# Kernel tuning notes

Measured on AMD Instinct MI355X. Metric: run time of the kernel, lower is better.

Reference implementation:

```python
import jax, jax.numpy as jnp
import numpy as np

B, D, H, W = 16, 512, 32, 32
K = 2048            # n_codes
BETA = 0.25
DECAY = 0.99
EPS = 1e-5


def _l2norm(x):
    # matches F.normalize(x, dim=-1) with eps=1e-12
    n = jnp.linalg.norm(x, axis=-1, keepdims=True)
    return x / jnp.maximum(n, 1e-12)


def setup_inputs() -> dict:
    key = jax.random.key(0)
    k1, k2, k3, k4 = jax.random.split(key, 4)
    z = jax.random.normal(k1, (B, D, H, W), dtype=jnp.float32)
    embeddings = jax.random.normal(k2, (K, D), dtype=jnp.float32) * (1.0 / K)
    N_buf = jax.random.uniform(k3, (K,), dtype=jnp.float32) + 0.5
    z_avg = jax.random.normal(k4, (K, D), dtype=jnp.float32) * (1.0 / K)
    return {"z": z, "embeddings": embeddings, "N_buf": N_buf, "z_avg": z_avg}


def reference(z, embeddings, N_buf, z_avg):
    b, d, h, w = z.shape
    # [B,C,H,W] -> [B,H,W,C] -> [N, D]
    flat = z.transpose(0, 2, 3, 1).reshape(-1, d)          # [N, D]
    z_norm = _l2norm(flat)                                  # [N, D]
    cb_norm = _l2norm(embeddings)                           # [K, D]

    # squared euclidean distances (kept in the same expanded form as source)
    distances = (jnp.sum(z_norm ** 2, axis=1, keepdims=True)
                 + jnp.sum(cb_norm ** 2, axis=1)
                 - 2.0 * jnp.matmul(z_norm, cb_norm.T))     # [N, K]
    distance_prob = jax.nn.softmax(-distances, axis=1)      # [N, K]
    encoding_indices = jnp.argmin(distances, axis=1)        # [N] int

    # NOTE: faithful to source -- gathers rows of z_norm (inputs), not codebook
    emb = z_norm[encoding_indices]                          # [N, D]

    # training-mode EMA statistics (one-hot matmul expressed as segment_sum)
    n_total = jax.ops.segment_sum(jnp.ones_like(encoding_indices, dtype=z.dtype),
                                  encoding_indices, num_segments=K)      # [K]
    encode_sum = jax.ops.segment_sum(z_norm, encoding_indices,
                                     num_segments=K)                     # [K, D]
    N_new = DECAY * N_buf + (1.0 - DECAY) * n_total
    z_avg_new = DECAY * z_avg + (1.0 - DECAY) * encode_sum
    n = jnp.sum(N_new)
    weights = (N_new + EPS) / (n + K * EPS) * n                          # [K]
    embeddings_new = z_avg_new / weights[:, None]                        # [K, D]

    commitment_loss = jnp.mean((z_norm - jax.lax.stop_gradient(emb)) ** 2)
    loss = BETA * commitment_loss
    codebook_sum = jnp.sum(jnp.abs(embeddings_new))

    q = emb.reshape(b, h, w, d).transpose(0, 3, 1, 2)       # [B, D, H, W]
    return (q, distance_prob, commitment_loss, loss, codebook_sum,
            embeddings_new, N_new, z_avg_new)
```

## Files before the change

### kernel.cpp

```cpp
#include <hip/hip_runtime.h>

#define NROW 16384
#define KC   2048
#define DIM  512

typedef __attribute__((ext_vector_type(8))) short  short8;
typedef __attribute__((ext_vector_type(4))) float  floatx4;


__device__ __forceinline__ unsigned short f2bf(float f) {
  unsigned int u = __float_as_uint(f);
  u += 0x7fffu + ((u >> 16) & 1u);
  return (unsigned short)(u >> 16);
}

#define GLDS(gsrc, ldst) __builtin_amdgcn_global_load_lds( \
    (const __attribute__((address_space(1))) unsigned int*)(gsrc), \
    (__attribute__((address_space(3))) unsigned int*)(ldst), 16, 0, 0)

__global__ void k_cbnorm(const float* __restrict__ emb,
                         unsigned short* __restrict__ cb_bf,
                         float* __restrict__ csq) {
  const int k = blockIdx.x;
  const int t = threadIdx.x;
  const float* row = emb + (size_t)k * DIM;
  float v0 = row[t], v1 = row[t + 256];
  float ss = v0 * v0 + v1 * v1;
#pragma unroll
  for (int o = 32; o; o >>= 1) ss += __shfl_xor(ss, o, 64);
  __shared__ float red[4];
  if ((t & 63) == 0) red[t >> 6] = ss;
  __syncthreads();
  float tot = red[0] + red[1] + red[2] + red[3];
  float r = 1.0f / fmaxf(sqrtf(tot), 1e-12f);
  cb_bf[(size_t)k * DIM + t]       = f2bf(v0 * r);
  cb_bf[(size_t)k * DIM + t + 256] = f2bf(v1 * r);
  if (t == 0) csq[k] = tot * r * r;
}

__global__ void k_pnorm(const float* __restrict__ z, float* __restrict__ rnorm) {
  const int b  = blockIdx.x;
  const int pc = blockIdx.y;
  const int tx = threadIdx.x & 63;
  const int ty = threadIdx.x >> 6;
  const int p  = pc * 64 + tx;
  const float* zp = z + (size_t)b * (DIM * 1024) + p;
  float ss = 0.f;
  for (int d = ty; d < DIM; d += 4) {
    float v = zp[(size_t)d * 1024];
    ss += v * v;
  }
  __shared__ float red[4][64];
  red[ty][tx] = ss;
  __syncthreads();
  if (ty == 0) {
    float tot = red[0][tx] + red[1][tx] + red[2][tx] + red[3][tx];
    rnorm[b * 1024 + p] = 1.0f / fmaxf(sqrtf(tot), 1e-12f);
  }
}

__global__ void k_transpose(const float* __restrict__ z, const float* __restrict__ rnorm,
                            float* __restrict__ flatT, unsigned short* __restrict__ zbf) {
  __shared__ float tile[32][33];
  __shared__ float srn[32];
  const int dt = blockIdx.x;
  const int pt = blockIdx.y;
  const int b  = blockIdx.z;
  const int tx = threadIdx.x & 31;
  const int ty = threadIdx.x >> 5;
  if (threadIdx.x < 32) srn[threadIdx.x] = rnorm[b * 1024 + pt * 32 + threadIdx.x];
  const size_t zb = (size_t)b * (DIM * 1024);
#pragma unroll
  for (int i = 0; i < 4; ++i) {
    int d = dt * 32 + ty + i * 8;
    int p = pt * 32 + tx;
    tile[ty + i * 8][tx] = z[zb + (size_t)d * 1024 + p];
  }
  __syncthreads();
#pragma unroll
  for (int i = 0; i < 4; ++i) {
    int p = pt * 32 + ty + i * 8;
    int d = dt * 32 + tx;
    float v = tile[tx][ty + i * 8];
    size_t o = (size_t)(b * 1024 + p) * DIM + d;
    flatT[o] = v;
    zbf[o]   = f2bf(v * srn[ty + i * 8]);
  }
}

__global__ __launch_bounds__(256) void k_gemm(const unsigned short* __restrict__ A,
                                              const unsigned short* __restrict__ Bm,
                                              const float* __restrict__ csq,
                                              float* __restrict__ T) {
  __shared__ alignas(16) unsigned short smA[128 * 64];
  __shared__ alignas(16) unsigned short smB[128 * 64];
  const int tid  = threadIdx.x;
  const int wid  = tid >> 6;
  const int lane = tid & 63;
  const int m0 = blockIdx.x * 128;
  const int n0 = blockIdx.y * 128;
  const int wm = (wid >> 1) * 64;
  const int wn = (wid & 1) * 64;

  floatx4 acc[4][4];
  const floatx4 z4 = {0.f, 0.f, 0.f, 0.f};
#pragma unroll
  for (int mi = 0; mi < 4; ++mi)
#pragma unroll
    for (int ni = 0; ni < 4; ++ni) acc[mi][ni] = z4;

  const int srow = tid >> 3;
  const int scol = (tid & 7) * 8;
  const unsigned short* Abase = A  + (size_t)(m0 + srow) * DIM + scol;
  const unsigned short* Bbase = Bm + (size_t)(n0 + srow) * DIM + scol;

  for (int kt = 0; kt < 8; ++kt) {
    const int kb = kt * 64;
#pragma unroll
    for (int i = 0; i < 4; ++i) {
      GLDS(Abase + kb + (size_t)i * 32 * DIM, &smA[i * 2048 + tid * 8]);
      GLDS(Bbase + kb + (size_t)i * 32 * DIM, &smB[i * 2048 + tid * 8]);
    }
    __syncthreads();
    const int q  = lane >> 4;
    const int mr = lane & 15;
#pragma unroll
    for (int kk = 0; kk < 2; ++kk) {
      const int cb = (kk * 4 + q) * 8;
      short8 af[4], bfr[4];
#pragma unroll
      for (int mi = 0; mi < 4; ++mi)
        af[mi] = *(const short8*)&smA[(wm + mi * 16 + mr) * 64 + cb];
#pragma unroll
      for (int ni = 0; ni < 4; ++ni)
        bfr[ni] = *(const short8*)&smB[(wn + ni * 16 + mr) * 64 + cb];
#pragma unroll
      for (int mi = 0; mi < 4; ++mi)
#pragma unroll
        for (int ni = 0; ni < 4; ++ni)
          acc[mi][ni] = __builtin_amdgcn_mfma_f32_16x16x32_bf16(af[mi], bfr[ni], acc[mi][ni], 0, 0, 0);
    }
    __syncthreads();
  }

  const int col = lane & 15;
  const int rq  = (lane >> 4) * 4;
  float csqv[4];
#pragma unroll
  for (int ni = 0; ni < 4; ++ni) csqv[ni] = csq[n0 + wn + ni * 16 + col];
#pragma unroll
  for (int mi = 0; mi < 4; ++mi)
#pragma unroll
    for (int r = 0; r < 4; ++r) {
      size_t rowoff = (size_t)(m0 + wm + mi * 16 + rq + r) * KC;
#pragma unroll
      for (int ni = 0; ni < 4; ++ni)
        T[rowoff + n0 + wn + ni * 16 + col] = 2.0f * acc[mi][ni][r] - csqv[ni];
    }
}

#define MARGIN_T 2.0e-2f

__global__ void k_row(float* __restrict__ T, const float* __restrict__ flatT,
                      const float* __restrict__ emb, const float* __restrict__ rnorm,
                      int* __restrict__ idx, float* __restrict__ enc_sum,
                      float* __restrict__ n_total, double* __restrict__ cl_part) {
  const int n = blockIdx.x;
  const int t = threadIdx.x;
  const int lane = t & 63;
  const int wid  = t >> 6;
  float* row = T + (size_t)n * KC;

  float tv[8];
  float mx = -3.4e38f;
#pragma unroll
  for (int j = 0; j < 8; ++j) {
    tv[j] = row[t + j * 256];
    mx = fmaxf(mx, tv[j]);
  }
#pragma unroll
  for (int o = 32; o; o >>= 1) mx = fmaxf(mx, __shfl_xor(mx, o, 64));
  __shared__ float redm[4];
  __shared__ float redsum[4];
  __shared__ int   s_cnt;
  __shared__ int   s_list[16];
  __shared__ int   s_j;
  if (t == 0) s_cnt = 0;
  if (lane == 0) redm[wid] = mx;
  __syncthreads();
  const float MX = fmaxf(fmaxf(redm[0], redm[1]), fmaxf(redm[2], redm[3]));
  float ev[8];
  float sum = 0.f;
#pragma unroll
  for (int j = 0; j < 8; ++j) {
    int k = t + j * 256;
    if (tv[j] >= MX - MARGIN_T) {
      int p = atomicAdd(&s_cnt, 1);
      if (p < 16) s_list[p] = k;
    }
    ev[j] = __expf(tv[j] - MX);
    sum += ev[j];
  }
#pragma unroll
  for (int o = 32; o; o >>= 1) sum += __shfl_xor(sum, o, 64);
  if (lane == 0) redsum[wid] = sum;
  __syncthreads();
  const float inv = 1.0f / (redsum[0] + redsum[1] + redsum[2] + redsum[3]);
#pragma unroll
  for (int j = 0; j < 8; ++j) row[t + j * 256] = ev[j] * inv;

  const int c = s_cnt;
  if (c == 1) {
    if (t == 0) s_j = s_list[0];
  } else if (wid == 0) {
    const float* zr = flatT + (size_t)n * DIM;
    double zs = 0.0;
    for (int d = lane; d < DIM; d += 64) { double v = zr[d]; zs += v * v; }
#pragma unroll
    for (int o = 32; o; o >>= 1) zs += __shfl_xor(zs, o, 64);
    double zn = fmax(sqrt(zs), 1e-12);
    double best = 1e300;
    int bestk = 0x7fffffff;
    const int m = (c > 16) ? KC : c;
    for (int ci = 0; ci < m; ++ci) {
      int k = (c > 16) ? ci : s_list[ci];
      const float* er = emb + (size_t)k * DIM;
      double cs = 0.0, dot = 0.0;
      for (int d = lane; d < DIM; d += 64) {
        double e = er[d], zv = zr[d];
        cs += e * e; dot += zv * e;
      }
#pragma unroll
      for (int o = 32; o; o >>= 1) { cs += __shfl_xor(cs, o, 64); dot += __shfl_xor(dot, o, 64); }
      double cn = fmax(sqrt(cs), 1e-12);
      double score = cs / (cn * cn) - 2.0 * dot / (zn * cn);
      if (score < best || (score == best && k < bestk)) { best = score; bestk = k; }
    }
    if (lane == 0) s_j = bestk;
  }
  __syncthreads();
  const int j = s_j;
  if (t == 0) idx[n] = j;

  const float rn = rnorm[n], rj = rnorm[j];
  const float* zr  = flatT + (size_t)n * DIM;
  const float* zjr = flatT + (size_t)j * DIM;
  double cl = 0.0;
#pragma unroll
  for (int i = 0; i < 2; ++i) {
    int d = t + i * 256;
    float zv  = zr[d] * rn;
    float evv = zjr[d] * rj;
    float df  = zv - evv;
    cl += (double)df * (double)df;
    atomicAdd(&enc_sum[(size_t)j * DIM + d], zv);
  }
#pragma unroll
  for (int o = 32; o; o >>= 1) cl += __shfl_xor(cl, o, 64);
  __shared__ double redd[4];
  if (lane == 0) redd[wid] = cl;
  __syncthreads();
  if (t == 0) {
    cl_part[n] = redd[0] + redd[1] + redd[2] + redd[3];
    atomicAdd(&n_total[j], 1.0f);
  }
}

__global__ void k_tail(const float* __restrict__ za, const float* __restrict__ es,
                       const float* __restrict__ Nb, const float* __restrict__ ntot,
                       float* __restrict__ out_zav, float* __restrict__ outN,
                       float* __restrict__ out_emb, double* __restrict__ cbs_part) {
  const int k = blockIdx.x;
  const int t = threadIdx.x;
  const int lane = t & 63, wid = t >> 6;
  float s = 0.f;
#pragma unroll
  for (int i = 0; i < 8; ++i) {
    int kk = t + i * 256;
    s += 0.99f * Nb[kk] + 0.01f * ntot[kk];
  }
#pragma unroll
  for (int o = 32; o; o >>= 1) s += __shfl_xor(s, o, 64);
  __shared__ float redn[4];
  if (lane == 0) redn[wid] = s;
  __syncthreads();
  const float nv = redn[0] + redn[1] + redn[2] + redn[3];
  const float Nn = 0.99f * Nb[k] + 0.01f * ntot[k];
  if (t == 0) outN[k] = Nn;
  const float w = (Nn + 1e-5f) / (nv + 0.02048f) * nv;
  double a = 0.0;
#pragma unroll
  for (int i = 0; i < 2; ++i) {
    size_t gi = (size_t)k * DIM + t + i * 256;
    float zv = 0.99f * za[gi] + 0.01f * es[gi];
    out_zav[gi] = zv;
    float e = zv / w;
    out_emb[gi] = e;
    a += (double)fabsf(e);
  }
#pragma unroll
  for (int o = 32; o; o >>= 1) a += __shfl_xor(a, o, 64);
  __shared__ double red[4];
  if (lane == 0) red[wid] = a;
  __syncthreads();
  if (t == 0) cbs_part[k] = red[0] + red[1] + red[2] + red[3];
}

__global__ void k_q(const float* __restrict__ flatT, const float* __restrict__ rnorm,
                    const int* __restrict__ idx, float* __restrict__ q) {
  const int o = blockIdx.x * 256 + threadIdx.x;
  const int b = o >> 19;
  const int d = (o >> 10) & 511;
  const int p = o & 1023;
  const int j = idx[(b << 10) + p];
  q[o] = flatT[(size_t)j * DIM + d] * rnorm[j];
}

__global__ void k_final(const double* __restrict__ cl_part, const double* __restrict__ cbs_part,
                        float* __restrict__ out) {
  const int t = threadIdx.x;
  double cl = 0.0, cb = 0.0;
  for (int i = t; i < NROW; i += 256) cl += cl_part[i];
  for (int i = t; i < KC; i += 256) cb += cbs_part[i];
#pragma unroll
  for (int o = 32; o; o >>= 1) { cl += __shfl_xor(cl, o, 64); cb += __shfl_xor(cb, o, 64); }
  __shared__ double redc[4], redb[4];
  if ((t & 63) == 0) { redc[t >> 6] = cl; redb[t >> 6] = cb; }
  __syncthreads();
  if (t == 0) {
    double clm = (redc[0] + redc[1] + redc[2] + redc[3]) / 8388608.0;
    double cbs = redb[0] + redb[1] + redb[2] + redb[3];
    out[41943040] = (float)clm;
    out[41943041] = (float)(0.25 * clm);
    out[41943042] = (float)cbs;
  }
}

extern "C" void kernel_launch(void* const* d_in, const int* in_sizes, int n_in,
                              void* d_out, int out_size, void* d_ws, size_t ws_size,
                              hipStream_t stream) {
  const float* z   = (const float*)d_in[0];
  const float* emb = (const float*)d_in[1];
  const float* Nb  = (const float*)d_in[2];
  const float* za  = (const float*)d_in[3];
  float* out = (float*)d_out;
  char*  ws  = (char*)d_ws;

  float*          flatT     = (float*)(ws + 0);
  unsigned short* cb_bf     = (unsigned short*)(ws + 33554432);
  float*          csq       = (float*)(ws + 35651584);
  float*          rnorm     = (float*)(ws + 35659776);
  int*            idx       = (int*)(ws + 35725312);
  double*         cl_part   = (double*)(ws + 35790848);
  double*         cbs_part  = (double*)(ws + 35921920);
  float*          enc_sum   = (float*)(ws + 35938304);
  float*          n_total   = (float*)(ws + 40132608);

  unsigned short* z_bf  = (unsigned short*)out;
  float* S        = out + 8388608;
  float* out_emb  = out + 41943043;
  float* out_N    = out + 42991619;
  float* out_zav  = out + 42993667;

  hipMemsetAsync(ws + 35938304, 0, 4202496, stream);

  k_cbnorm   <<<KC, 256, 0, stream>>>(emb, cb_bf, csq);
  k_pnorm    <<<dim3(16, 16), 256, 0, stream>>>(z, rnorm);
  k_transpose<<<dim3(16, 32, 16), 256, 0, stream>>>(z, rnorm, flatT, z_bf);
  k_gemm     <<<dim3(NROW / 128, KC / 128), 256, 0, stream>>>(z_bf, cb_bf, csq, S);
  k_row      <<<NROW, 256, 0, stream>>>(S, flatT, emb, rnorm, idx, enc_sum, n_total, cl_part);
  k_tail     <<<KC, 256, 0, stream>>>(za, enc_sum, Nb, n_total, out_zav, out_N, out_emb, cbs_part);
  k_q        <<<32768, 256, 0, stream>>>(flatT, rnorm, idx, out);
  k_final    <<<1, 256, 0, stream>>>(cl_part, cbs_part, out);
}
```

Measured before the change: 468.1 us.

## Use fixed softmax shift, split row kernel, merge small kernels

The softmax kernel now exponentiates with a fixed shift of 1, relying on normalized vectors bounding logits, so max and sum reduce together in one pass with vectorized float4 loads and stores. Candidate selection uses a multiplicative threshold on exponentials and writes candidates to global memory. A separate pick kernel then handles argmin refinement and accumulation. The codebook and pixel norm kernels are merged into one launch, and the final reduction is folded into an extra block of the q kernel. This trades one extra launch and extra global traffic for fewer barriers and better-coalesced softmax access.

```diff
diff --git a/kernel.cpp b/kernel.cpp
--- a/kernel.cpp
+++ b/kernel.cpp
@@ -18,44 +18,47 @@
     (const __attribute__((address_space(1))) unsigned int*)(gsrc), \
     (__attribute__((address_space(3))) unsigned int*)(ldst), 16, 0, 0)
 
-__global__ void k_cbnorm(const float* __restrict__ emb,
-                         unsigned short* __restrict__ cb_bf,
-                         float* __restrict__ csq) {
-  const int k = blockIdx.x;
-  const int t = threadIdx.x;
-  const float* row = emb + (size_t)k * DIM;
-  float v0 = row[t], v1 = row[t + 256];
-  float ss = v0 * v0 + v1 * v1;
-#pragma unroll
-  for (int o = 32; o; o >>= 1) ss += __shfl_xor(ss, o, 64);
-  __shared__ float red[4];
-  if ((t & 63) == 0) red[t >> 6] = ss;
-  __syncthreads();
-  float tot = red[0] + red[1] + red[2] + red[3];
-  float r = 1.0f / fmaxf(sqrtf(tot), 1e-12f);
-  cb_bf[(size_t)k * DIM + t]       = f2bf(v0 * r);
-  cb_bf[(size_t)k * DIM + t + 256] = f2bf(v1 * r);
-  if (t == 0) csq[k] = tot * r * r;
-}
-
-__global__ void k_pnorm(const float* __restrict__ z, float* __restrict__ rnorm) {
-  const int b  = blockIdx.x;
-  const int pc = blockIdx.y;
-  const int tx = threadIdx.x & 63;
-  const int ty = threadIdx.x >> 6;
-  const int p  = pc * 64 + tx;
-  const float* zp = z + (size_t)b * (DIM * 1024) + p;
-  float ss = 0.f;
-  for (int d = ty; d < DIM; d += 4) {
-    float v = zp[(size_t)d * 1024];
-    ss += v * v;
-  }
-  __shared__ float red[4][64];
-  red[ty][tx] = ss;
-  __syncthreads();
-  if (ty == 0) {
-    float tot = red[0][tx] + red[1][tx] + red[2][tx] + red[3][tx];
-    rnorm[b * 1024 + p] = 1.0f / fmaxf(sqrtf(tot), 1e-12f);
+__global__ void k_prep(const float* __restrict__ emb,
+                       unsigned short* __restrict__ cb_bf,
+                       float* __restrict__ csq,
+                       const float* __restrict__ z,
+                       float* __restrict__ rnorm) {
+  __shared__ float red4[4];
+  __shared__ float redp[4][64];
+  if (blockIdx.x < KC) {
+    const int k = blockIdx.x;
+    const int t = threadIdx.x;
+    const float* row = emb + (size_t)k * DIM;
+    float v0 = row[t], v1 = row[t + 256];
+    float ss = v0 * v0 + v1 * v1;
+#pragma unroll
+    for (int o = 32; o; o >>= 1) ss += __shfl_xor(ss, o, 64);
+    if ((t & 63) == 0) red4[t >> 6] = ss;
+    __syncthreads();
+    float tot = red4[0] + red4[1] + red4[2] + red4[3];
+    float r = 1.0f / fmaxf(sqrtf(tot), 1e-12f);
+    cb_bf[(size_t)k * DIM + t]       = f2bf(v0 * r);
+    cb_bf[(size_t)k * DIM + t + 256] = f2bf(v1 * r);
+    if (t == 0) csq[k] = tot * r * r;
+  } else {
+    const int blk = blockIdx.x - KC;
+    const int b  = blk >> 4;
+    const int pc = blk & 15;
+    const int tx = threadIdx.x & 63;
+    const int ty = threadIdx.x >> 6;
+    const int p  = pc * 64 + tx;
+    const float* zp = z + (size_t)b * (DIM * 1024) + p;
+    float ss = 0.f;
+    for (int d = ty; d < DIM; d += 4) {
+      float v = zp[(size_t)d * 1024];
+      ss += v * v;
+    }
+    redp[ty][tx] = ss;
+    __syncthreads();
+    if (ty == 0) {
+      float tot = redp[0][tx] + redp[1][tx] + redp[2][tx] + redp[3][tx];
+      rnorm[b * 1024 + p] = 1.0f / fmaxf(sqrtf(tot), 1e-12f);
+    }
   }
 }
 
@@ -159,59 +162,69 @@
     }
 }
 
-#define MARGIN_T 2.0e-2f
-
-__global__ void k_row(float* __restrict__ T, const float* __restrict__ flatT,
-                      const float* __restrict__ emb, const float* __restrict__ rnorm,
-                      int* __restrict__ idx, float* __restrict__ enc_sum,
-                      float* __restrict__ n_total, double* __restrict__ cl_part) {
+#define EXP_MARGIN 0.980198673f
+
+__global__ void k_softmax(float* __restrict__ T,
+                          int* __restrict__ cand_cnt, int* __restrict__ cand_list) {
   const int n = blockIdx.x;
   const int t = threadIdx.x;
-  const int lane = t & 63;
-  const int wid  = t >> 6;
+  const int lane = t & 63, wid = t >> 6;
   float* row = T + (size_t)n * KC;
-
-  float tv[8];
-  float mx = -3.4e38f;
+  floatx4 v0 = *(const floatx4*)&row[t * 8];
+  floatx4 v1 = *(const floatx4*)&row[t * 8 + 4];
+  float ev[8];
+  float mx = 0.f, sum = 0.f;
+#pragma unroll
+  for (int j = 0; j < 4; ++j) {
+    ev[j]     = __expf(v0[j] - 1.0f);
+    ev[j + 4] = __expf(v1[j] - 1.0f);
+  }
 #pragma unroll
   for (int j = 0; j < 8; ++j) {
-    tv[j] = row[t + j * 256];
-    mx = fmaxf(mx, tv[j]);
-  }
-#pragma unroll
-  for (int o = 32; o; o >>= 1) mx = fmaxf(mx, __shfl_xor(mx, o, 64));
-  __shared__ float redm[4];
-  __shared__ float redsum[4];
-  __shared__ int   s_cnt;
-  __shared__ int   s_list[16];
-  __shared__ int   s_j;
+    mx = fmaxf(mx, ev[j]);
+    sum += ev[j];
+  }
+#pragma unroll
+  for (int o = 32; o; o >>= 1) {
+    mx  = fmaxf(mx, __shfl_xor(mx, o, 64));
+    sum += __shfl_xor(sum, o, 64);
+  }
+  __shared__ float redm[4], reds[4];
+  __shared__ int s_cnt;
   if (t == 0) s_cnt = 0;
-  if (lane == 0) redm[wid] = mx;
-  __syncthreads();
-  const float MX = fmaxf(fmaxf(redm[0], redm[1]), fmaxf(redm[2], redm[3]));
-  float ev[8];
-  float sum = 0.f;
+  if (lane == 0) { redm[wid] = mx; reds[wid] = sum; }
+  __syncthreads();
+  const float EMX = fmaxf(fmaxf(redm[0], redm[1]), fmaxf(redm[2], redm[3]));
+  const float inv = 1.0f / (reds[0] + reds[1] + reds[2] + reds[3]);
+  const float thr = EMX * EXP_MARGIN;
 #pragma unroll
   for (int j = 0; j < 8; ++j) {
-    int k = t + j * 256;
-    if (tv[j] >= MX - MARGIN_T) {
+    if (ev[j] >= thr) {
       int p = atomicAdd(&s_cnt, 1);
-      if (p < 16) s_list[p] = k;
-    }
-    ev[j] = __expf(tv[j] - MX);
-    sum += ev[j];
-  }
-#pragma unroll
-  for (int o = 32; o; o >>= 1) sum += __shfl_xor(sum, o, 64);
-  if (lane == 0) redsum[wid] = sum;
-  __syncthreads();
-  const float inv = 1.0f / (redsum[0] + redsum[1] + redsum[2] + redsum[3]);
-#pragma unroll
-  for (int j = 0; j < 8; ++j) row[t + j * 256] = ev[j] * inv;
-
-  const int c = s_cnt;
+      if (p < 16) cand_list[n * 16 + p] = t * 8 + j;
+    }
+  }
+  floatx4 w0, w1;
+#pragma unroll
+  for (int j = 0; j < 4; ++j) { w0[j] = ev[j] * inv; w1[j] = ev[j + 4] * inv; }
+  *(floatx4*)&row[t * 8]     = w0;
+  *(floatx4*)&row[t * 8 + 4] = w1;
+  __syncthreads();
+  if (t == 0) cand_cnt[n] = (s_cnt > 16) ? -1 : s_cnt;
+}
+
+__global__ void k_pick(const float* __restrict__ flatT, const float* __restrict__ emb,
+                       const float* __restrict__ rnorm,
+                       const int* __restrict__ cand_cnt, const int* __restrict__ cand_list,
+                       int* __restrict__ idx, float* __restrict__ enc_sum,
+                       float* __restrict__ n_total, double* __restrict__ cl_part) {
+  const int n = blockIdx.x;
+  const int t = threadIdx.x;
+  const int lane = t & 63, wid = t >> 6;
+  __shared__ int s_j;
+  const int c = cand_cnt[n];
   if (c == 1) {
-    if (t == 0) s_j = s_list[0];
+    if (t == 0) s_j = cand_list[n * 16];
   } else if (wid == 0) {
     const float* zr = flatT + (size_t)n * DIM;
     double zs = 0.0;
@@ -221,9 +234,9 @@
     double zn = fmax(sqrt(zs), 1e-12);
     double best = 1e300;
     int bestk = 0x7fffffff;
-    const int m = (c > 16) ? KC : c;
+    const int m = (c < 0) ? KC : c;
     for (int ci = 0; ci < m; ++ci) {
-      int k = (c > 16) ? ci : s_list[ci];
+      int k = (c < 0) ? ci : cand_list[n * 16 + ci];
       const float* er = emb + (size_t)k * DIM;
       double cs = 0.0, dot = 0.0;
       for (int d = lane; d < DIM; d += 64) {
@@ -307,33 +320,33 @@
 }
 
 __global__ void k_q(const float* __restrict__ flatT, const float* __restrict__ rnorm,
-                    const int* __restrict__ idx, float* __restrict__ q) {
+                    const int* __restrict__ idx, float* __restrict__ out,
+                    const double* __restrict__ cl_part, const double* __restrict__ cbs_part) {
+  if (blockIdx.x == 32768) {
+    const int t = threadIdx.x;
+    double cl = 0.0, cb = 0.0;
+    for (int i = t; i < NROW; i += 256) cl += cl_part[i];
+    for (int i = t; i < KC; i += 256) cb += cbs_part[i];
+#pragma unroll
+    for (int o = 32; o; o >>= 1) { cl += __shfl_xor(cl, o, 64); cb += __shfl_xor(cb, o, 64); }
+    __shared__ double redc[4], redb[4];
+    if ((t & 63) == 0) { redc[t >> 6] = cl; redb[t >> 6] = cb; }
+    __syncthreads();
+    if (t == 0) {
+      double clm = (redc[0] + redc[1] + redc[2] + redc[3]) / 8388608.0;
+      double cbs = redb[0] + redb[1] + redb[2] + redb[3];
+      out[41943040] = (float)clm;
+      out[41943041] = (float)(0.25 * clm);
+      out[41943042] = (float)cbs;
+    }
+    return;
+  }
   const int o = blockIdx.x * 256 + threadIdx.x;
   const int b = o >> 19;
   const int d = (o >> 10) & 511;
   const int p = o & 1023;
   const int j = idx[(b << 10) + p];
-  q[o] = flatT[(size_t)j * DIM + d] * rnorm[j];
-}
-
-__global__ void k_final(const double* __restrict__ cl_part, const double* __restrict__ cbs_part,
-                        float* __restrict__ out) {
-  const int t = threadIdx.x;
-  double cl = 0.0, cb = 0.0;
-  for (int i = t; i < NROW; i += 256) cl += cl_part[i];
-  for (int i = t; i < KC; i += 256) cb += cbs_part[i];
-#pragma unroll
-  for (int o = 32; o; o >>= 1) { cl += __shfl_xor(cl, o, 64); cb += __shfl_xor(cb, o, 64); }
-  __shared__ double redc[4], redb[4];
-  if ((t & 63) == 0) { redc[t >> 6] = cl; redb[t >> 6] = cb; }
-  __syncthreads();
-  if (t == 0) {
-    double clm = (redc[0] + redc[1] + redc[2] + redc[3]) / 8388608.0;
-    double cbs = redb[0] + redb[1] + redb[2] + redb[3];
-    out[41943040] = (float)clm;
-    out[41943041] = (float)(0.25 * clm);
-    out[41943042] = (float)cbs;
-  }
+  out[o] = flatT[(size_t)j * DIM + d] * rnorm[j];
 }
 
 extern "C" void kernel_launch(void* const* d_in, const int* in_sizes, int n_in,
@@ -351,10 +364,12 @@
   float*          csq       = (float*)(ws + 35651584);
   float*          rnorm     = (float*)(ws + 35659776);
   int*            idx       = (int*)(ws + 35725312);
-  double*         cl_part   = (double*)(ws + 35790848);
-  double*         cbs_part  = (double*)(ws + 35921920);
-  float*          enc_sum   = (float*)(ws + 35938304);
-  float*          n_total   = (float*)(ws + 40132608);
+  int*            cand_cnt  = (int*)(ws + 35790848);
+  int*            cand_list = (int*)(ws + 35856384);
+  double*         cl_part   = (double*)(ws + 36904960);
+  double*         cbs_part  = (double*)(ws + 37036032);
+  float*          enc_sum   = (float*)(ws + 37052416);
+  float*          n_total   = (float*)(ws + 41246720);
 
   unsigned short* z_bf  = (unsigned short*)out;
   float* S        = out + 8388608;
@@ -362,14 +377,13 @@
   float* out_N    = out + 42991619;
   float* out_zav  = out + 42993667;
 
-  hipMemsetAsync(ws + 35938304, 0, 4202496, stream);
-
-  k_cbnorm   <<<KC, 256, 0, stream>>>(emb, cb_bf, csq);
-  k_pnorm    <<<dim3(16, 16), 256, 0, stream>>>(z, rnorm);
+  hipMemsetAsync(ws + 37052416, 0, 4202496, stream);
+
+  k_prep     <<<KC + 256, 256, 0, stream>>>(emb, cb_bf, csq, z, rnorm);
   k_transpose<<<dim3(16, 32, 16), 256, 0, stream>>>(z, rnorm, flatT, z_bf);
   k_gemm     <<<dim3(NROW / 128, KC / 128), 256, 0, stream>>>(z_bf, cb_bf, csq, S);
-  k_row      <<<NROW, 256, 0, stream>>>(S, flatT, emb, rnorm, idx, enc_sum, n_total, cl_part);
+  k_softmax  <<<NROW, 256, 0, stream>>>(S, cand_cnt, cand_list);
+  k_pick     <<<NROW, 256, 0, stream>>>(flatT, emb, rnorm, cand_cnt, cand_list, idx, enc_sum, n_total, cl_part);
   k_tail     <<<KC, 256, 0, stream>>>(za, enc_sum, Nb, n_total, out_zav, out_N, out_emb, cbs_part);
-  k_q        <<<32768, 256, 0, stream>>>(flatT, rnorm, idx, out);
-  k_final    <<<1, 256, 0, stream>>>(cl_part, cbs_part, out);
-}
+  k_q        <<<32769, 256, 0, stream>>>(flatT, rnorm, idx, out, cl_part, cbs_part);
+}
```

Measured after the change: 490.4 us. 1.05x slower.
